# Performance work log

Hardware: AMD Instinct MI355X
Metric: run time of the kernel (lower is better)

Reference implementation:

```python
import jax, jax.numpy as jnp
import numpy as np

R = 32  # voxel resolution
B, CIN, COUT, N = 4, 64, 64, 4096
K = 3


def setup_inputs():
    key = jax.random.key(0)
    ks = jax.random.split(key, 8)
    s = 0.05
    return {
        "features": jax.random.normal(ks[0], (B, CIN, N), jnp.float32),
        "coords": jax.random.normal(ks[1], (B, 3, N), jnp.float32),
        # voxel branch: conv3d + BN x2
        "w1": jax.random.normal(ks[2], (COUT, CIN, K, K, K), jnp.float32) * s,
        "b1": jnp.zeros((COUT,), jnp.float32),
        "g1": jnp.ones((COUT,), jnp.float32),
        "be1": jnp.zeros((COUT,), jnp.float32),
        "w2": jax.random.normal(ks[3], (COUT, COUT, K, K, K), jnp.float32) * s,
        "b2": jnp.zeros((COUT,), jnp.float32),
        "g2": jnp.ones((COUT,), jnp.float32),
        "be2": jnp.zeros((COUT,), jnp.float32),
        # point branch SharedMLP (1x1 conv + BN + ReLU)
        "wp": jax.random.normal(ks[4], (COUT, CIN), jnp.float32) * s,
        "bp": jnp.zeros((COUT,), jnp.float32),
        "gp": jnp.ones((COUT,), jnp.float32),
        "bep": jnp.zeros((COUT,), jnp.float32),
        # fuzzy_proj 1x1 conv
        "wf": jax.random.normal(ks[5], (COUT, CIN), jnp.float32) * s,
        "bf": jnp.zeros((COUT,), jnp.float32),
        # fusion SharedMLP (3*COUT -> COUT)
        "wfu": jax.random.normal(ks[6], (COUT, 3 * COUT), jnp.float32) * s,
        "bfu": jnp.zeros((COUT,), jnp.float32),
        "gfu": jnp.ones((COUT,), jnp.float32),
        "befu": jnp.zeros((COUT,), jnp.float32),
    }


def _bn3d(x, g, b):
    # training-mode BatchNorm3d, eps=1e-4 (biased variance, as torch)
    m = x.mean((0, 2, 3, 4), keepdims=True)
    v = x.var((0, 2, 3, 4), keepdims=True)
    return (x - m) * jax.lax.rsqrt(v + 1e-4) * g[None, :, None, None, None] + b[None, :, None, None, None]


def _bn1d(x, g, b):
    m = x.mean((0, 2), keepdims=True)
    v = x.var((0, 2), keepdims=True)
    return (x - m) * jax.lax.rsqrt(v + 1e-4) * g[None, :, None] + b[None, :, None]


def _conv3d(x, w, b):
    pad = K // 2
    y = jax.lax.conv_general_dilated(x, w, (1, 1, 1), [(pad, pad)] * 3,
                                     dimension_numbers=('NCDHW', 'OIDHW', 'NCDHW'))
    return y + b[None, :, None, None, None]


def _conv1x1(x, w, b):
    return jnp.einsum('oc,bcn->bon', w, x) + b[None, :, None]


def _voxelize(features, coords):
    # PVCNN Voxelization(normalize=True, eps=0): center, scale to unit, grid coords in [0, R-1]
    nc = coords - coords.mean(axis=2, keepdims=True)              # [B,3,N]
    norm = jnp.linalg.norm(nc, axis=1, keepdims=True)             # [B,1,N]
    nc = nc / (norm.max(axis=2, keepdims=True) * 2.0) + 0.5
    nc = jnp.clip(nc * R, 0.0, R - 1)
    vox = jnp.round(nc).astype(jnp.int32)                         # [B,3,N]
    b_, c_, n_ = features.shape
    idx = (vox[:, 0] * R + vox[:, 1]) * R + vox[:, 2]             # [B,N]
    flat = (idx + jnp.arange(b_)[:, None] * R ** 3).reshape(-1)
    feat = features.transpose(0, 2, 1).reshape(b_ * n_, c_)
    sums = jax.ops.segment_sum(feat, flat, num_segments=b_ * R ** 3)
    cnt = jax.ops.segment_sum(jnp.ones((b_ * n_,), feat.dtype), flat, num_segments=b_ * R ** 3)
    avg = sums / jnp.maximum(cnt, 1.0)[:, None]                   # scatter-mean
    grid = avg.reshape(b_, R ** 3, c_).transpose(0, 2, 1).reshape(b_, c_, R, R, R)
    return grid, nc


def _devoxelize(grid, nc):
    # trilinear gather: grid [B,C,R,R,R], nc [B,3,N] float coords in [0,R-1]
    b_, c_ = grid.shape[:2]
    g = grid.reshape(b_, c_, -1)
    lo_f = jnp.floor(nc)
    fr = nc - lo_f                                                # fractional part [B,3,N]
    lo = lo_f.astype(jnp.int32)
    hi = jnp.minimum(lo + 1, R - 1)
    out = jnp.zeros((b_, c_, nc.shape[2]), grid.dtype)
    for dx in (0, 1):
        for dy in (0, 1):
            for dz in (0, 1):
                ix = hi[:, 0] if dx else lo[:, 0]
                iy = hi[:, 1] if dy else lo[:, 1]
                iz = hi[:, 2] if dz else lo[:, 2]
                w = ((fr[:, 0] if dx else 1.0 - fr[:, 0]) *
                     (fr[:, 1] if dy else 1.0 - fr[:, 1]) *
                     (fr[:, 2] if dz else 1.0 - fr[:, 2]))        # [B,N]
                flat = (ix * R + iy) * R + iz                     # [B,N]
                vals = jnp.take_along_axis(g, flat[:, None, :], axis=2)  # [B,C,N]
                out = out + vals * w[:, None, :]
    return out


def reference(features, coords, w1, b1, g1, be1, w2, b2, g2, be2,
              wp, bp, gp, bep, wf, bf, wfu, bfu, gfu, befu):
    lrelu = lambda x: jnp.where(x > 0, x, 0.1 * x)
    # voxel branch
    grid, nc = _voxelize(features, coords)
    v = lrelu(_bn3d(_conv3d(grid, w1, b1), g1, be1))
    v = lrelu(_bn3d(_conv3d(v, w2, b2), g2, be2))
    vox_feat = _devoxelize(v, nc)                                 # [B,COUT,N]
    # point branch
    pt = jax.nn.relu(_bn1d(_conv1x1(features, wp, bp), gp, bep))
    # fuzzy branch: dense attention over points
    cn = coords.transpose(0, 2, 1)                                # [B,N,3]
    cn = cn / jnp.maximum(jnp.linalg.norm(cn, axis=-1, keepdims=True), 1e-12)
    att = jax.nn.softmax(jnp.einsum('bnd,bmd->bnm', cn, cn) / 0.1, axis=-1)
    fz = jnp.einsum('bnm,bcm->bcn', att, features)                # [B,CIN,N]
    fz = _conv1x1(fz, wf, bf)
    # fusion
    comb = jnp.concatenate([vox_feat, pt, fz], axis=1)            # [B,3*COUT,N]
    fused = jax.nn.relu(_bn1d(_conv1x1(comb, wfu, bfu), gfu, befu))
    return (fused, coords)
```

## Files before the change

### kernel.cpp

```cpp
#include <hip/hip_runtime.h>
#include <hip/hip_bf16.h>
#include <math.h>

#define RR 32
#define R3 32768
#define BB 4
#define CI 64
#define CO 64
#define NN 4096

typedef short v8s __attribute__((ext_vector_type(8)));
typedef float v4f __attribute__((ext_vector_type(4)));
typedef unsigned short ushort_t;

__device__ __forceinline__ unsigned short f2bf(float f) {
    unsigned int u = __float_as_uint(f);
    unsigned int r = (u + 0x7FFFu + ((u >> 16) & 1u)) >> 16;
    return (unsigned short)r;
}
__device__ __forceinline__ float bf2f(unsigned short h) {
    return __uint_as_float((unsigned int)h << 16);
}

__device__ __forceinline__ void gll16(const void* g, void* l) {
// ... 126 lines not shown
    }
}

__global__ void k_scan1(const int* __restrict__ cntI, int* __restrict__ lscan,
                        int* __restrict__ bsum, int* __restrict__ rank) {
    __shared__ int sm[256];
    int tid = threadIdx.x;
    int i = blockIdx.x * 256 + tid;
    rank[i] = 0;
    int v = cntI[i];
    sm[tid] = v; __syncthreads();
    for (int off = 1; off < 256; off <<= 1) {
        int t = (tid >= off) ? sm[tid - off] : 0;
        __syncthreads();
        sm[tid] += t;
        __syncthreads();
    }
    lscan[i] = sm[tid] - v;
    if (tid == 255) bsum[blockIdx.x] = sm[tid];
}

__global__ void k_scan2(const int* __restrict__ bsum, int* __restrict__ bbase) {
    __shared__ int sm[512];
    int tid = threadIdx.x;
    int v = bsum[tid];
    sm[tid] = v; __syncthreads();
    for (int off = 1; off < 512; off <<= 1) {
        int t = (tid >= off) ? sm[tid - off] : 0;
        __syncthreads();
        sm[tid] += t;
        __syncthreads();
    }
    bbase[tid] = sm[tid] - v;
}

__global__ void k_fill(const int* __restrict__ vidx, const int* __restrict__ lscan,
                       const int* __restrict__ bbase, int* __restrict__ rank,
                       int* __restrict__ plist) {
    int i = blockIdx.x * 256 + threadIdx.x;
    int b = i >> 12, n = i & (NN - 1);
    int flat = b * R3 + vidx[i];
    int r = atomicAdd(&rank[flat], 1);
    plist[bbase[flat >> 8] + lscan[flat] + r] = n;
}

__global__ __launch_bounds__(256) void k_gather(const float* __restrict__ featT,
                                                const int* __restrict__ cntI,
                                                const int* __restrict__ lscan,
                                                const int* __restrict__ bbase,
                                                const int* __restrict__ plist,
                                                ushort_t* __restrict__ gT) {
    int wv = threadIdx.x >> 6, lane = threadIdx.x & 63;
    int vbase = blockIdx.x * 32 + wv * 8;
    for (int k = 0; k < 8; k++) {
        int flat = vbase + k;
        int count = cntI[flat];
        float s = 0.0f;
        if (count > 0) {
            int b = flat >> 15;
            int start = bbase[flat >> 8] + lscan[flat];
            for (int j = 0; j < count; j++) {
                int n = plist[start + j];
                s += featT[((size_t)b * NN + n) * 64 + lane];
            }
            s *= 1.0f / (float)count;
        }
        gT[(size_t)flat * 64 + lane] = f2bf(s);
    }
}

__global__ void k_bncast2(const ushort_t* __restrict__ x, const float* __restrict__ accs,
                          const float* __restrict__ g, const float* __restrict__ be,
                          float invcnt, float slope, ushort_t* __restrict__ o) {
    size_t i = (size_t)blockIdx.x * 256 + threadIdx.x;
    int c0 = (int)((i * 8) & 63);
    float sc[8], sh[8];
    #pragma unroll
    for (int j = 0; j < 8; j++) {
        int c = c0 + j;
        float mean = accs[2 * c] * invcnt;
        float var = accs[2 * c + 1] * invcnt - mean * mean;
        float scale = g[c] * rsqrtf(var + 1e-4f);
        sc[j] = scale;
        sh[j] = be[c] - mean * scale;
    }
    uint4 in = ((const uint4*)x)[i];
    unsigned iv[4] = {in.x, in.y, in.z, in.w};
    unsigned pk[4];
    #pragma unroll
    for (int j = 0; j < 4; j++) {
        float u0 = bf2f((unsigned short)(iv[j] & 0xFFFF)) * sc[2 * j] + sh[2 * j];
        float u1 = bf2f((unsigned short)(iv[j] >> 16)) * sc[2 * j + 1] + sh[2 * j + 1];
        u0 = u0 > 0 ? u0 : slope * u0;
        u1 = u1 > 0 ? u1 : slope * u1;
        pk[j] = (unsigned)f2bf(u0) | ((unsigned)f2bf(u1) << 16);
    }
    ((uint4*)o)[i] = make_uint4(pk[0], pk[1], pk[2], pk[3]);
}

template <int OUTBF16>
__global__ __launch_bounds__(256) void k_convlds(const ushort_t* __restrict__ gT,
                                                 const ushort_t* __restrict__ wS,
                                                 void* __restrict__ outP,
                                                 float* __restrict__ accs) {
    __shared__ ushort_t lin[20480];
    __shared__ ushort_t lw[2][6144];
    int bid = blockIdx.x;
    int wgid = (bid & 7) * 64 + (bid >> 3);
    int yt = wgid & 3, z0 = (wgid >> 2) & 31, b = wgid >> 7;
    int tid = threadIdx.x;
    int w = __builtin_amdgcn_readfirstlane(tid >> 6);
    int lane = tid & 63, l15 = lane & 15, l4 = lane >> 4;
    int y0 = yt * 8;
    const ushort_t* gTb = gT + (size_t)b * R3 * 64;

    int voxF[4];
    #pragma unroll
    for (int f = 0; f < 4; f++)
        voxF[f] = (w * 2 + (f >> 1)) * 32 + (f & 1) * 16 + l15 - 1;
    bool xlo_ok = (l15 != 0), xhi_ok = (l15 != 15);

    int lsw = lane ^ ((lane >> 3) & 7);
    int wsz8 = ((l15 * 4 + l4) ^ ((l15 >> 1) & 7)) * 8;

    const v8s vzero = {};
    v4f acc[4][4];
    #pragma unroll
    for (int m = 0; m < 4; m++)
        #pragma unroll
        for (int f = 0; f < 4; f++)
            acc[m][f] = (v4f){0.0f, 0.0f, 0.0f, 0.0f};

#define WSTAGE(s)                                                              \
    do {                                                                       \
        const ushort_t* _src = wS + (size_t)(s) * 6144;                        \
        ushort_t* _dst = lw[(s) & 1];                                          \
        _Pragma("unroll") for (int _i = 0; _i < 3; _i++) {                     \
            int _pb = _i * 256 + w * 64;                                       \
            gll16(_src + (size_t)(_pb + lsw) * 8, _dst + (size_t)(_pb + lane) * 8); \
        }                                                                      \
    } while (0)

#define ISTAGE(dz)                                                             \
    do {                                                                       \
        int _zp = z0 - 1 + (dz);                                               \
        if (_zp < 0 || _zp > 31) {                                             \
            for (int _q = 0; _q < 10; _q++)                                    \
                *(v8s*)&lin[(size_t)(w * 640 + _q * 64 + lane) * 8] = vzero;   \
        } else {                                                               \
            if (yt == 0) *(v8s*)&lin[(size_t)tid * 8] = vzero;                 \
            if (yt == 3) *(v8s*)&lin[(size_t)(2304 + tid) * 8] = vzero;        \
            const ushort_t* _pb = gTb + ((size_t)_zp * 1024 + (size_t)(y0 - 1) * 32) * 64; \
            int _g0 = (yt == 0) ? 256 : 0;                                     \
            int _nc = 10 - (yt == 0) - (yt == 3);                              \
            for (int _i = 0; _i < _nc; _i++) {                                 \
                int _pbase = _g0 + _i * 256 + w * 64;                          \
                int _p = _pbase + lane;                                        \
                int _vx = _p >> 3, _js = _p & 7;                               \
                int _sg = _vx * 8 + (_js ^ (_vx & 7));                         \
                gll16(_pb + (size_t)_sg * 8, lin + (size_t)_pbase * 8);        \
            }                                                                  \
        }                                                                      \
    } while (0)

    WSTAGE(0);
    for (int s = 0; s < 18; s++) {
        int dy = (s / 2) % 3, cih = s & 1;
        asm volatile("s_barrier" ::: "memory");
        if ((s % 6) == 0) ISTAGE(s / 6);
        if (s + 1 < 18) WSTAGE(s + 1);
        if (s + 1 < 18) asm volatile("s_waitcnt vmcnt(3) lgkmcnt(0)" ::: "memory");
        else            asm volatile("s_waitcnt vmcnt(0) lgkmcnt(0)" ::: "memory");
        asm volatile("s_barrier" ::: "memory");

        const ushort_t* lwb = lw[s & 1];
        #pragma unroll
        for (int dx = 0; dx < 3; dx++) {
            v8s Bf[4];
            #pragma unroll
            for (int f = 0; f < 4; f++) {
                int vox = voxF[f] + dy * 32 + dx;
                int g = vox * 8 + ((cih * 4 + l4) ^ (vox & 7));
                int bix = g * 16;
                bix = bix < 0 ? 0 : bix;
                v8s vb = *(const v8s*)((const char*)lin + bix);
                bool ok = (dx == 0 && (f & 1) == 0) ? xlo_ok :
                          (dx == 2 && (f & 1) == 1) ? xhi_ok : true;
                Bf[f] = ok ? vb : vzero;
            }
            const ushort_t* ap = lwb + dx * 2048 + wsz8;
            #pragma unroll
            for (int m = 0; m < 4; m++) {
                v8s Af = *(const v8s*)(ap + m * 512);
                #pragma unroll
                for (int f = 0; f < 4; f++)
                    acc[m][f] = __builtin_amdgcn_mfma_f32_16x16x32_bf16(Af, Bf[f], acc[m][f], 0, 0, 0);
            }
        }
    }

    #pragma unroll
    for (int m = 0; m < 4; m++) {
        #pragma unroll
        for (int f = 0; f < 4; f++) {
            int y = y0 + w * 2 + (f >> 1);
            int x = (f & 1) * 16 + l15;
            size_t base = ((size_t)b * R3 + z0 * 1024 + y * 32 + x) * 64 + m * 16 + l4 * 4;
            if (OUTBF16) {
                unsigned p0 = (unsigned)f2bf(acc[m][f][0]) | ((unsigned)f2bf(acc[m][f][1]) << 16);
                unsigned p1 = (unsigned)f2bf(acc[m][f][2]) | ((unsigned)f2bf(acc[m][f][3]) << 16);
                *(uint2*)&((ushort_t*)outP)[base] = make_uint2(p0, p1);
            } else {
                float4 o = make_float4(acc[m][f][0], acc[m][f][1], acc[m][f][2], acc[m][f][3]);
                *(float4*)&((float*)outP)[base] = o;
            }
        }
    }

    __syncthreads();
    float* sbuf = (float*)lin;
    #pragma unroll
    for (int m = 0; m < 4; m++)
        #pragma unroll
        for (int r = 0; r < 4; r++) {
            float s = 0, q = 0;
            #pragma unroll
            for (int f = 0; f < 4; f++) {
                float v = acc[m][f][r];
                s += v; q += v * v;
            }
            sbuf[tid * 33 + (m * 4 + r) * 2] = s;
            sbuf[tid * 33 + (m * 4 + r) * 2 + 1] = q;
        }
    __syncthreads();
    if (tid < 128) {
        int co = tid >> 1, val = tid & 1;
        int m = co >> 4, cl4 = (co >> 2) & 3, r = co & 3;
        float a = 0;
        for (int w2 = 0; w2 < 4; w2++)
            for (int l = 0; l < 16; l++)
                a += sbuf[(w2 * 64 + cl4 * 16 + l) * 33 + (m * 4 + r) * 2 + val];
        atomicAdd(&accs[2 * co + val], a);
    }
#undef WSTAGE
#undef ISTAGE
}

__global__ void k_bnfin2(const float* __restrict__ pst, const float* __restrict__ g,
                         const float* __restrict__ be, float* __restrict__ stats,
                         float invcnt) {
    int c = blockIdx.x, tid = threadIdx.x;
    __shared__ float rs[256], rq[256];
    rs[tid] = pst[(c * 256 + tid) * 2];
    rq[tid] = pst[(c * 256 + tid) * 2 + 1];
    __syncthreads();
    for (int off = 128; off > 0; off >>= 1) {
        if (tid < off) { rs[tid] += rs[tid + off]; rq[tid] += rq[tid + off]; }
        __syncthreads();
    }
    if (tid == 0) {
        float mean = rs[0] * invcnt;
        float var = rq[0] * invcnt - mean * mean;
        float sc = g[c] * rsqrtf(var + 1e-4f);
        stats[2 * c] = sc;
        stats[2 * c + 1] = be[c] - mean * sc;
    }
}

__global__ void k_bnact2(const float* __restrict__ x, const float* __restrict__ pst,
                         const float* __restrict__ g, const float* __restrict__ be,
                         float invcnt, float* __restrict__ out) {
    int bid = blockIdx.x, tid = threadIdx.x;
    int c = (bid >> 2) & 63;
    __shared__ float rs[256], rq[256];
    __shared__ float sscale, sshift;
    rs[tid] = pst[(c * 256 + tid) * 2];
    rq[tid] = pst[(c * 256 + tid) * 2 + 1];
    __syncthreads();
    for (int off = 128; off > 0; off >>= 1) {
        if (tid < off) { rs[tid] += rs[tid + off]; rq[tid] += rq[tid + off]; }
        __syncthreads();
    }
    if (tid == 0) {
        float mean = rs[0] * invcnt;
        float var = rq[0] * invcnt - mean * mean;
        float sc = g[c] * rsqrtf(var + 1e-4f);
        sscale = sc;
        sshift = be[c] - mean * sc;
    }
    __syncthreads();
    float sc = sscale, sh = sshift;
    size_t i = (size_t)bid * 256 + tid;
    float4 v = ((const float4*)x)[i];
    v.x = fmaxf(v.x * sc + sh, 0.0f);
    v.y = fmaxf(v.y * sc + sh, 0.0f);
    v.z = fmaxf(v.z * sc + sh, 0.0f);
    v.w = fmaxf(v.w * sc + sh, 0.0f);
    ((float4*)out)[i] = v;
}

__global__ void k_devox2(const ushort_t* __restrict__ gcl, const float* __restrict__ accs,
                         const float* __restrict__ g, const float* __restrict__ be,
                         float invcnt, const float* __restrict__ nc,
                         float* __restrict__ out) {
    int b = blockIdx.y;
    int tid = threadIdx.x, p = tid >> 4, q = tid & 15;
    int n = blockIdx.x * 16 + p;
    float x = nc[((size_t)b * 3 + 0) * NN + n];
    float y = nc[((size_t)b * 3 + 1) * NN + n];
    float z = nc[((size_t)b * 3 + 2) * NN + n];
    float fx = floorf(x), fy = floorf(y), fz = floorf(z);
    int lx = (int)fx, ly = (int)fy, lz = (int)fz;
    int hx = min(lx + 1, RR - 1), hy = min(ly + 1, RR - 1), hz = min(lz + 1, RR - 1);
    float frx = x - fx, fry = y - fy, frz = z - fz;
    int xx[2] = {lx, hx}, yy[2] = {ly, hy}, zz[2] = {lz, hz};
    float wx[2] = {1.0f - frx, frx}, wy[2] = {1.0f - fry, fry}, wz[2] = {1.0f - frz, frz};
    float sc[4], sh[4];
    #pragma unroll
    for (int j = 0; j < 4; j++) {
        int c = q * 4 + j;
        float mean = accs[2 * c] * invcnt;
        float var = accs[2 * c + 1] * invcnt - mean * mean;
        float scale = g[c] * rsqrtf(var + 1e-4f);
        sc[j] = scale;
        sh[j] = be[c] - mean * scale;
    }
    float a0 = 0, a1 = 0, a2 = 0, a3 = 0;
    #pragma unroll
    for (int dx = 0; dx < 2; dx++)
        #pragma unroll
        for (int dy = 0; dy < 2; dy++)
            #pragma unroll
            for (int dz = 0; dz < 2; dz++) {
                int idx = (xx[dx] * RR + yy[dy]) * RR + zz[dz];
                float wt = wx[dx] * wy[dy] * wz[dz];
                uint2 pv = *(const uint2*)&gcl[((size_t)b * R3 + idx) * 64 + q * 4];
                float v0 = bf2f((unsigned short)(pv.x & 0xFFFF));
                float v1 = bf2f((unsigned short)(pv.x >> 16));
                float v2 = bf2f((unsigned short)(pv.y & 0xFFFF));
                float v3 = bf2f((unsigned short)(pv.y >> 16));
                float u0 = v0 * sc[0] + sh[0]; u0 = u0 > 0 ? u0 : 0.1f * u0;
                float u1 = v1 * sc[1] + sh[1]; u1 = u1 > 0 ? u1 : 0.1f * u1;
                float u2 = v2 * sc[2] + sh[2]; u2 = u2 > 0 ? u2 : 0.1f * u2;
                float u3 = v3 * sc[3] + sh[3]; u3 = u3 > 0 ? u3 : 0.1f * u3;
                a0 += wt * u0; a1 += wt * u1; a2 += wt * u2; a3 += wt * u3;
            }
    out[((size_t)(b * 64 + q * 4 + 0)) * NN + n] = a0;
    out[((size_t)(b * 64 + q * 4 + 1)) * NN + n] = a1;
    out[((size_t)(b * 64 + q * 4 + 2)) * NN + n] = a2;
    out[((size_t)(b * 64 + q * 4 + 3)) * NN + n] = a3;
}

__global__ __launch_bounds__(256) void k_fuzzym(const float* __restrict__ coords,
                                                const ushort_t* __restrict__ featb,
                                                float* __restrict__ pnum,
                                                float* __restrict__ pden) {
    __shared__ float cm[3][1024];
    __shared__ ushort_t la[4][2048];
    int b = blockIdx.z, mc = blockIdx.y, nt = blockIdx.x;
    int tid = threadIdx.x;
    int w = tid >> 6, lane = tid & 63, l15 = lane & 15, l4 = lane >> 4;
    int m0 = mc * 1024;

    for (int i = tid; i < 1024; i += 256) {
        float a0 = coords[((size_t)b * 3 + 0) * NN + m0 + i];
        float a1 = coords[((size_t)b * 3 + 1) * NN + m0 + i];
        float a2 = coords[((size_t)b * 3 + 2) * NN + m0 + i];
        float inv = 1.0f / fmaxf(sqrtf(a0 * a0 + a1 * a1 + a2 * a2), 1e-12f);
        cm[0][i] = a0 * inv; cm[1][i] = a1 * inv; cm[2][i] = a2 * inv;
    }

    int n = nt * 64 + w * 16 + l15;
    float q0 = coords[((size_t)b * 3 + 0) * NN + n];
    float q1 = coords[((size_t)b * 3 + 1) * NN + n];
    float q2 = coords[((size_t)b * 3 + 2) * NN + n];
    float qi = 10.0f / fmaxf(sqrtf(q0 * q0 + q1 * q1 + q2 * q2), 1e-12f);
    q0 *= qi; q1 *= qi; q2 *= qi;

    int srow = tid >> 2, sslot = tid & 3;
    int g0 = sslot ^ ((srow >> 1) & 3);
    const ushort_t* fb = featb + (size_t)b * 64 * NN + m0;
    const ushort_t* sbase = fb + (size_t)srow * NN + g0 * 8;
    int rsw = (l15 >> 1) & 3;

    v4f acc[4];
    #pragma unroll
    for (int cb = 0; cb < 4; cb++) acc[cb] = (v4f){0.0f, 0.0f, 0.0f, 0.0f};
    float den = 0.0f;

    gll16(sbase, &la[0][(size_t)tid * 8]);
    gll16(sbase + 32, &la[1][(size_t)tid * 8]);
    gll16(sbase + 64, &la[2][(size_t)tid * 8]);

    for (int t = 0; t < 32; t++) {
        int cur = t & 3;
        asm volatile("s_waitcnt vmcnt(2)" ::: "memory");
        __syncthreads();
        if (t + 3 < 32)
            gll16(sbase + (t + 3) * 32, &la[(t + 3) & 3][(size_t)tid * 8]);

        int mo = t * 32 + l4 * 8;
        float e[8];
        #pragma unroll
        for (int jj = 0; jj < 2; jj++) {
            float4 x0 = *(const float4*)&cm[0][mo + jj * 4];
            float4 x1 = *(const float4*)&cm[1][mo + jj * 4];
            float4 x2 = *(const float4*)&cm[2][mo + jj * 4];
            e[jj * 4 + 0] = __expf(q0 * x0.x + q1 * x1.x + q2 * x2.x);
            e[jj * 4 + 1] = __expf(q0 * x0.y + q1 * x1.y + q2 * x2.y);
            e[jj * 4 + 2] = __expf(q0 * x0.z + q1 * x1.z + q2 * x2.z);
            e[jj * 4 + 3] = __expf(q0 * x0.w + q1 * x1.w + q2 * x2.w);
        }
        den += ((e[0] + e[1]) + (e[2] + e[3])) + ((e[4] + e[5]) + (e[6] + e[7]));
        union { __hip_bfloat162 h[4]; v8s v; } pk;
        pk.h[0] = __float22bfloat162_rn(make_float2(e[0], e[1]));
        pk.h[1] = __float22bfloat162_rn(make_float2(e[2], e[3]));
        pk.h[2] = __float22bfloat162_rn(make_float2(e[4], e[5]));
        pk.h[3] = __float22bfloat162_rn(make_float2(e[6], e[7]));
        #pragma unroll
        for (int cb = 0; cb < 4; cb++) {
            v8s A = *(const v8s*)&la[cur][(size_t)((cb * 16 + l15) * 4 + (l4 ^ rsw)) * 8];
            acc[cb] = __builtin_amdgcn_mfma_f32_16x16x32_bf16(A, pk.v, acc[cb], 0, 0, 0);
        }
    }

    den += __shfl_xor(den, 16);
    den += __shfl_xor(den, 32);

    size_t obase = ((size_t)(b * 4 + mc)) * 64 * NN;
    #pragma unroll
    for (int cb = 0; cb < 4; cb++)
        #pragma unroll
        for (int r = 0; r < 4; r++)
            pnum[obase + (size_t)(cb * 16 + l4 * 4 + r) * NN + n] = acc[cb][r];
    if (l4 == 0) pden[((size_t)(b * 4 + mc)) * NN + n] = den;
}

__global__ void k_combine2(const float* __restrict__ pnum, const float* __restrict__ pden,
                           float* __restrict__ fzf) {
    int i4 = blockIdx.x * 256 + threadIdx.x;
    int b = i4 >> 16, c = (i4 >> 10) & 63, n4 = i4 & 1023;
    float4 num = make_float4(0, 0, 0, 0), den = make_float4(0, 0, 0, 0);
    #pragma unroll
    for (int ch = 0; ch < 4; ch++) {
        float4 pn = ((const float4*)pnum)[((size_t)(b * 4 + ch) * 64 + c) * 1024 + n4];
        float4 pd = ((const float4*)pden)[(size_t)(b * 4 + ch) * 1024 + n4];
        num.x += pn.x; num.y += pn.y; num.z += pn.z; num.w += pn.w;
        den.x += pd.x; den.y += pd.y; den.z += pd.z; den.w += pd.w;
    }
    float4 o = make_float4(num.x / den.x, num.y / den.y, num.z / den.z, num.w / den.w);
    ((float4*)fzf)[((size_t)(b * 64 + c)) * 1024 + n4] = o;
}

__global__ __launch_bounds__(256) void k_1x1s(const float* __restrict__ in,
                                              const float* __restrict__ wT,
                                              const float* __restrict__ bias,
                                              float* __restrict__ out,
                                              float* __restrict__ pst) {
    int b = blockIdx.z, ob = blockIdx.y, bx = blockIdx.x;
    int tid = threadIdx.x;
    int q = tid & 15, o = ob * 16 + (tid >> 4);
    int n = bx * 64 + q * 4;
    const float* src = in + (size_t)b * 64 * NN + n;
    const float* wp_ = wT + o;
    v4f acc = {0, 0, 0, 0};
    #pragma unroll 8
    for (int c = 0; c < 64; c++) {
        float4 x = *(const float4*)&src[(size_t)c * NN];
        float w = wp_[c * 64];
        acc[0] += x.x * w; acc[1] += x.y * w; acc[2] += x.z * w; acc[3] += x.w * w;
    }
    float bv = bias[o];
    float s = 0, q2 = 0;
    float4 ov;
    float* op = (float*)&ov;
    #pragma unroll
    for (int v = 0; v < 4; v++) {
        float val = acc[v] + bv;
        op[v] = val;
        s += val; q2 += val * val;
    }
    *(float4*)&out[((size_t)(b * 64 + o)) * NN + n] = ov;
    #pragma unroll
    for (int off = 1; off < 16; off <<= 1) {
        s += __shfl_xor(s, off);
        q2 += __shfl_xor(q2, off);
    }
    if (q == 0) {
        int part = bx * 4 + b;
        pst[(o * 256 + part) * 2] = s;
        pst[(o * 256 + part) * 2 + 1] = q2;
    }
}

__global__ __launch_bounds__(256) void k_1x1f(const float* __restrict__ vox,
                                              const float* __restrict__ pt,
                                              const float* __restrict__ fzf,
                                              const float* __restrict__ bnB,
                                              const float* __restrict__ wfuT,
                                              const float* __restrict__ bC,
                                              float* __restrict__ out,
                                              float* __restrict__ pst) {
    int b = blockIdx.z, ob = blockIdx.y, bx = blockIdx.x;
    int tid = threadIdx.x;
    int q = tid & 15, o = ob * 16 + (tid >> 4);
    int n = bx * 64 + q * 4;
    const float* srcA = vox + (size_t)b * 64 * NN + n;
    const float* srcB = pt + (size_t)b * 64 * NN + n;
    const float* srcC = fzf + (size_t)b * 64 * NN + n;
    const float* wA = wfuT + o;
    v4f acc = {0, 0, 0, 0};
    #pragma unroll 8
    for (int c = 0; c < 64; c++) {
        float4 x = *(const float4*)&srcA[(size_t)c * NN];
        float w = wA[c * 64];
        acc[0] += x.x * w; acc[1] += x.y * w; acc[2] += x.z * w; acc[3] += x.w * w;
    }
    #pragma unroll 8
    for (int c = 0; c < 64; c++) {
        float4 x = *(const float4*)&srcB[(size_t)c * NN];
        float sc = bnB[2 * c], sh = bnB[2 * c + 1];
        float w = wA[(64 + c) * 64];
        float x0 = fmaxf(x.x * sc + sh, 0.0f), x1 = fmaxf(x.y * sc + sh, 0.0f);
        float x2 = fmaxf(x.z * sc + sh, 0.0f), x3 = fmaxf(x.w * sc + sh, 0.0f);
        acc[0] += x0 * w; acc[1] += x1 * w; acc[2] += x2 * w; acc[3] += x3 * w;
    }
    #pragma unroll 8
    for (int c = 0; c < 64; c++) {
        float4 x = *(const float4*)&srcC[(size_t)c * NN];
        float w = wA[(128 + c) * 64];
        acc[0] += x.x * w; acc[1] += x.y * w; acc[2] += x.z * w; acc[3] += x.w * w;
    }
    float bv = bC[o];
    float s = 0, q2 = 0;
    float4 ov;
    float* op = (float*)&ov;
    #pragma unroll
    for (int v = 0; v < 4; v++) {
        float val = acc[v] + bv;
        op[v] = val;
        s += val; q2 += val * val;
    }
    *(float4*)&out[((size_t)(b * 64 + o)) * NN + n] = ov;
    #pragma unroll
    for (int off = 1; off < 16; off <<= 1) {
        s += __shfl_xor(s, off);
        q2 += __shfl_xor(q2, off);
    }
    if (q == 0) {
        int part = bx * 4 + b;
        pst[(o * 256 + part) * 2] = s;
        pst[(o * 256 + part) * 2 + 1] = q2;
    }
}

extern "C" void kernel_launch(void* const* d_in, const int* in_sizes, int n_in,
                              void* d_out, int out_size, void* d_ws, size_t ws_size,
                              hipStream_t stream) {
    const float* features = (const float*)d_in[0];
    const float* coords = (const float*)d_in[1];
    const float* w1 = (const float*)d_in[2];
    const float* g1 = (const float*)d_in[4];
    const float* be1 = (const float*)d_in[5];
    const float* w2 = (const float*)d_in[6];
    const float* g2 = (const float*)d_in[8];
    const float* be2 = (const float*)d_in[9];
    const float* wp = (const float*)d_in[10];
    const float* bp = (const float*)d_in[11];
    const float* gp = (const float*)d_in[12];
    const float* bep = (const float*)d_in[13];
    const float* wf = (const float*)d_in[14];
    const float* bf = (const float*)d_in[15];
    const float* wfu = (const float*)d_in[16];
    const float* bfu = (const float*)d_in[17];
    const float* gfu = (const float*)d_in[18];
    const float* befu = (const float*)d_in[19];

    float* ws = (float*)d_ws;
    float* nc = ws;
    int* vidx = (int*)(ws + 49152);
    int* cntI = (int*)(ws + 65536);
    float* pden = ws + 65536;
    float* gridCL = ws + 196608;
    ushort_t* gTraw = (ushort_t*)gridCL;
    int* rank = (int*)(ws + 196608);
    int* lscan = (int*)(ws + 327680);
    int* bsum = (int*)(ws + 458752);
    int* bbase = (int*)(ws + 459264);
    int* plist = (int*)(ws + 459776);
    float* featT = ws + 476160;
    float* gTpool = ws + 8585216;
    ushort_t* gT = (ushort_t*)gTpool;
    float* pnum = gTpool;
    float* pstB = gTpool + 4194304;
    float* stats = ws + 16973824;
    float* voxreg = ws + 16974336;
    ushort_t* wS1 = (ushort_t*)voxreg;
    ushort_t* wS2 = wS1 + 110592;
    float* vox = voxreg;
    float* pt = ws + 18022912;
    float* fzf = ws + 19071488;
    float* wpT = ws + 20120064;
    float* wfuT = wpT + 4096;
    float* bC = wfuT + 12288;
    float* fpre = ws + 21168640;
    ushort_t* featb = (ushort_t*)fpre;
    float* accs = ws + 22217216;

    float* out = (float*)d_out;

    k_prep<<<1699, 256, 0, stream>>>(wp, wfu, wf, bf, bfu, wpT, wfuT, bC, accs,
                                     w1, w2, wS1, wS2, features, featT, featb, cntI);

    k_nc<<<BB, 256, 0, stream>>>(coords, nc, vidx, cntI);
    k_scan1<<<512, 256, 0, stream>>>(cntI, lscan, bsum, rank);
    k_scan2<<<1, 512, 0, stream>>>(bsum, bbase);
    k_fill<<<BB * NN / 256, 256, 0, stream>>>(vidx, lscan, bbase, rank, plist);
    k_gather<<<4096, 256, 0, stream>>>(featT, cntI, lscan, bbase, plist, gT);

    k_convlds<1><<<512, 256, 0, stream>>>(gT, wS1, gTraw, accs);
    k_bncast2<<<BB * R3 * 64 / 8 / 256, 256, 0, stream>>>(gTraw, accs, g1, be1,
                                                          1.0f / (BB * R3), 0.1f, gT);
    k_convlds<1><<<512, 256, 0, stream>>>(gT, wS2, gTraw, accs + 128);
    k_devox2<<<dim3(NN / 16, BB), 256, 0, stream>>>(gTraw, accs + 128, g2, be2,
                                                    1.0f / (BB * R3), nc, vox);

    k_fuzzym<<<dim3(64, 4, BB), 256, 0, stream>>>(coords, featb, pnum, pden);
    k_combine2<<<BB * 64 * NN / 4 / 256, 256, 0, stream>>>(pnum, pden, fzf);

    k_1x1s<<<dim3(NN / 64, 4, BB), 256, 0, stream>>>(features, wpT, bp, pt, pstB);
    k_bnfin2<<<64, 256, 0, stream>>>(pstB, gp, bep, stats + 256, 1.0f / (BB * NN));

    k_1x1f<<<dim3(NN / 64, 4, BB), 256, 0, stream>>>(vox, pt, fzf, stats + 256, wfuT, bC,
                                                     fpre, pstB);
    k_bnact2<<<BB * 64 * NN / 4 / 256, 256, 0, stream>>>(fpre, pstB, gfu, befu,
                                                         1.0f / (BB * NN), out);

    hipMemcpyAsync(out + (size_t)BB * CO * NN, coords, (size_t)BB * 3 * NN * 4,
                   hipMemcpyDeviceToDevice, stream);
}
```

Measured before the change: 256.6 us.

## Merge independent mid-stage kernels into block-dispatched launches and fold coords copy

Devoxelize, fuzzy attention and point-branch 1x1 conv are merged into one launch that picks its branch from the block index. Fuzzy combine and point BN finalize share another launch, and the coords output copy moves into the final BN-activation kernel in place of a separate memcpy. This removes several launch gaps and lets the independent branches run concurrently on the GPU. The cost is a uniform shared-memory allocation across all branches, which can lower occupancy for the lighter branches, plus uneven work per block.

Measured after the change: 237.3 us. 1.08x faster.

```diff
diff --git a/kernel.cpp b/kernel.cpp
--- a/kernel.cpp
+++ b/kernel.cpp
@@ -302,7 +302,7 @@
             if (yt == 3) *(v8s*)&lin[(size_t)(2304 + tid) * 8] = vzero;        \
             const ushort_t* _pb = gTb + ((size_t)_zp * 1024 + (size_t)(y0 - 1) * 32) * 64; \
             int _g0 = (yt == 0) ? 256 : 0;                                     \
-            int _nc = 10 - (yt == 0) - (yt == 3);                              \
+            int _nc = 10 - (yt == 0) - (yt == 3);                               \
             for (int _i = 0; _i < _nc; _i++) {                                 \
                 int _pbase = _g0 + _i * 256 + w * 64;                          \
                 int _p = _pbase + lane;                                        \
@@ -396,250 +396,218 @@
 #undef ISTAGE
 }
 
-__global__ void k_bnfin2(const float* __restrict__ pst, const float* __restrict__ g,
-                         const float* __restrict__ be, float* __restrict__ stats,
-                         float invcnt) {
-    int c = blockIdx.x, tid = threadIdx.x;
-    __shared__ float rs[256], rq[256];
-    rs[tid] = pst[(c * 256 + tid) * 2];
-    rq[tid] = pst[(c * 256 + tid) * 2 + 1];
-    __syncthreads();
-    for (int off = 128; off > 0; off >>= 1) {
-        if (tid < off) { rs[tid] += rs[tid + off]; rq[tid] += rq[tid + off]; }
-        __syncthreads();
-    }
-    if (tid == 0) {
-        float mean = rs[0] * invcnt;
-        float var = rq[0] * invcnt - mean * mean;
-        float sc = g[c] * rsqrtf(var + 1e-4f);
-        stats[2 * c] = sc;
-        stats[2 * c + 1] = be[c] - mean * sc;
-    }
-}
-
-__global__ void k_bnact2(const float* __restrict__ x, const float* __restrict__ pst,
-                         const float* __restrict__ g, const float* __restrict__ be,
-                         float invcnt, float* __restrict__ out) {
-    int bid = blockIdx.x, tid = threadIdx.x;
-    int c = (bid >> 2) & 63;
-    __shared__ float rs[256], rq[256];
-    __shared__ float sscale, sshift;
-    rs[tid] = pst[(c * 256 + tid) * 2];
-    rq[tid] = pst[(c * 256 + tid) * 2 + 1];
-    __syncthreads();
-    for (int off = 128; off > 0; off >>= 1) {
-        if (tid < off) { rs[tid] += rs[tid + off]; rq[tid] += rq[tid + off]; }
-        __syncthreads();
-    }
-    if (tid == 0) {
-        float mean = rs[0] * invcnt;
-        float var = rq[0] * invcnt - mean * mean;
-        float sc = g[c] * rsqrtf(var + 1e-4f);
-        sscale = sc;
-        sshift = be[c] - mean * sc;
-    }
-    __syncthreads();
-    float sc = sscale, sh = sshift;
-    size_t i = (size_t)bid * 256 + tid;
-    float4 v = ((const float4*)x)[i];
-    v.x = fmaxf(v.x * sc + sh, 0.0f);
-    v.y = fmaxf(v.y * sc + sh, 0.0f);
-    v.z = fmaxf(v.z * sc + sh, 0.0f);
-    v.w = fmaxf(v.w * sc + sh, 0.0f);
-    ((float4*)out)[i] = v;
-}
-
-__global__ void k_devox2(const ushort_t* __restrict__ gcl, const float* __restrict__ accs,
-                         const float* __restrict__ g, const float* __restrict__ be,
-                         float invcnt, const float* __restrict__ nc,
-                         float* __restrict__ out) {
-    int b = blockIdx.y;
-    int tid = threadIdx.x, p = tid >> 4, q = tid & 15;
-    int n = blockIdx.x * 16 + p;
-    float x = nc[((size_t)b * 3 + 0) * NN + n];
-    float y = nc[((size_t)b * 3 + 1) * NN + n];
-    float z = nc[((size_t)b * 3 + 2) * NN + n];
-    float fx = floorf(x), fy = floorf(y), fz = floorf(z);
-    int lx = (int)fx, ly = (int)fy, lz = (int)fz;
-    int hx = min(lx + 1, RR - 1), hy = min(ly + 1, RR - 1), hz = min(lz + 1, RR - 1);
-    float frx = x - fx, fry = y - fy, frz = z - fz;
-    int xx[2] = {lx, hx}, yy[2] = {ly, hy}, zz[2] = {lz, hz};
-    float wx[2] = {1.0f - frx, frx}, wy[2] = {1.0f - fry, fry}, wz[2] = {1.0f - frz, frz};
-    float sc[4], sh[4];
-    #pragma unroll
-    for (int j = 0; j < 4; j++) {
-        int c = q * 4 + j;
-        float mean = accs[2 * c] * invcnt;
-        float var = accs[2 * c + 1] * invcnt - mean * mean;
-        float scale = g[c] * rsqrtf(var + 1e-4f);
-        sc[j] = scale;
-        sh[j] = be[c] - mean * scale;
-    }
-    float a0 = 0, a1 = 0, a2 = 0, a3 = 0;
-    #pragma unroll
-    for (int dx = 0; dx < 2; dx++)
-        #pragma unroll
-        for (int dy = 0; dy < 2; dy++)
-            #pragma unroll
-            for (int dz = 0; dz < 2; dz++) {
-                int idx = (xx[dx] * RR + yy[dy]) * RR + zz[dz];
-                float wt = wx[dx] * wy[dy] * wz[dz];
-                uint2 pv = *(const uint2*)&gcl[((size_t)b * R3 + idx) * 64 + q * 4];
-                float v0 = bf2f((unsigned short)(pv.x & 0xFFFF));
-                float v1 = bf2f((unsigned short)(pv.x >> 16));
-                float v2 = bf2f((unsigned short)(pv.y & 0xFFFF));
-                float v3 = bf2f((unsigned short)(pv.y >> 16));
-                float u0 = v0 * sc[0] + sh[0]; u0 = u0 > 0 ? u0 : 0.1f * u0;
-                float u1 = v1 * sc[1] + sh[1]; u1 = u1 > 0 ? u1 : 0.1f * u1;
-                float u2 = v2 * sc[2] + sh[2]; u2 = u2 > 0 ? u2 : 0.1f * u2;
-                float u3 = v3 * sc[3] + sh[3]; u3 = u3 > 0 ? u3 : 0.1f * u3;
-                a0 += wt * u0; a1 += wt * u1; a2 += wt * u2; a3 += wt * u3;
-            }
-    out[((size_t)(b * 64 + q * 4 + 0)) * NN + n] = a0;
-    out[((size_t)(b * 64 + q * 4 + 1)) * NN + n] = a1;
-    out[((size_t)(b * 64 + q * 4 + 2)) * NN + n] = a2;
-    out[((size_t)(b * 64 + q * 4 + 3)) * NN + n] = a3;
-}
-
-__global__ __launch_bounds__(256) void k_fuzzym(const float* __restrict__ coords,
-                                                const ushort_t* __restrict__ featb,
-                                                float* __restrict__ pnum,
-                                                float* __restrict__ pden) {
+__global__ __launch_bounds__(256) void k_mid(
+        const ushort_t* __restrict__ gcl, const float* __restrict__ accs2,
+        const float* __restrict__ g2, const float* __restrict__ be2, float invcntR3,
+        const float* __restrict__ nc, float* __restrict__ vox,
+        const float* __restrict__ coords, const ushort_t* __restrict__ featb,
+        float* __restrict__ pnum, float* __restrict__ pden,
+        const float* __restrict__ features, const float* __restrict__ wpT,
+        const float* __restrict__ bp, float* __restrict__ pt, float* __restrict__ pstB) {
     __shared__ float cm[3][1024];
     __shared__ ushort_t la[4][2048];
-    int b = blockIdx.z, mc = blockIdx.y, nt = blockIdx.x;
-    int tid = threadIdx.x;
-    int w = tid >> 6, lane = tid & 63, l15 = lane & 15, l4 = lane >> 4;
-    int m0 = mc * 1024;
-
-    for (int i = tid; i < 1024; i += 256) {
-        float a0 = coords[((size_t)b * 3 + 0) * NN + m0 + i];
-        float a1 = coords[((size_t)b * 3 + 1) * NN + m0 + i];
-        float a2 = coords[((size_t)b * 3 + 2) * NN + m0 + i];
-        float inv = 1.0f / fmaxf(sqrtf(a0 * a0 + a1 * a1 + a2 * a2), 1e-12f);
-        cm[0][i] = a0 * inv; cm[1][i] = a1 * inv; cm[2][i] = a2 * inv;
-    }
-
-    int n = nt * 64 + w * 16 + l15;
-    float q0 = coords[((size_t)b * 3 + 0) * NN + n];
-    float q1 = coords[((size_t)b * 3 + 1) * NN + n];
-    float q2 = coords[((size_t)b * 3 + 2) * NN + n];
-    float qi = 10.0f / fmaxf(sqrtf(q0 * q0 + q1 * q1 + q2 * q2), 1e-12f);
-    q0 *= qi; q1 *= qi; q2 *= qi;
-
-    int srow = tid >> 2, sslot = tid & 3;
-    int g0 = sslot ^ ((srow >> 1) & 3);
-    const ushort_t* fb = featb + (size_t)b * 64 * NN + m0;
-    const ushort_t* sbase = fb + (size_t)srow * NN + g0 * 8;
-    int rsw = (l15 >> 1) & 3;
-
-    v4f acc[4];
-    #pragma unroll
-    for (int cb = 0; cb < 4; cb++) acc[cb] = (v4f){0.0f, 0.0f, 0.0f, 0.0f};
-    float den = 0.0f;
-
-    gll16(sbase, &la[0][(size_t)tid * 8]);
-    gll16(sbase + 32, &la[1][(size_t)tid * 8]);
-    gll16(sbase + 64, &la[2][(size_t)tid * 8]);
-
-    for (int t = 0; t < 32; t++) {
-        int cur = t & 3;
-        asm volatile("s_waitcnt vmcnt(2)" ::: "memory");
-        __syncthreads();
-        if (t + 3 < 32)
-            gll16(sbase + (t + 3) * 32, &la[(t + 3) & 3][(size_t)tid * 8]);
-
-        int mo = t * 32 + l4 * 8;
-        float e[8];
-        #pragma unroll
-        for (int jj = 0; jj < 2; jj++) {
-            float4 x0 = *(const float4*)&cm[0][mo + jj * 4];
-            float4 x1 = *(const float4*)&cm[1][mo + jj * 4];
-            float4 x2 = *(const float4*)&cm[2][mo + jj * 4];
-            e[jj * 4 + 0] = __expf(q0 * x0.x + q1 * x1.x + q2 * x2.x);
-            e[jj * 4 + 1] = __expf(q0 * x0.y + q1 * x1.y + q2 * x2.y);
-            e[jj * 4 + 2] = __expf(q0 * x0.z + q1 * x1.z + q2 * x2.z);
-            e[jj * 4 + 3] = __expf(q0 * x0.w + q1 * x1.w + q2 * x2.w);
-        }
-        den += ((e[0] + e[1]) + (e[2] + e[3])) + ((e[4] + e[5]) + (e[6] + e[7]));
-        union { __hip_bfloat162 h[4]; v8s v; } pk;
-        pk.h[0] = __float22bfloat162_rn(make_float2(e[0], e[1]));
-        pk.h[1] = __float22bfloat162_rn(make_float2(e[2], e[3]));
-        pk.h[2] = __float22bfloat162_rn(make_float2(e[4], e[5]));
-        pk.h[3] = __float22bfloat162_rn(make_float2(e[6], e[7]));
-        #pragma unroll
-        for (int cb = 0; cb < 4; cb++) {
-            v8s A = *(const v8s*)&la[cur][(size_t)((cb * 16 + l15) * 4 + (l4 ^ rsw)) * 8];
-            acc[cb] = __builtin_amdgcn_mfma_f32_16x16x32_bf16(A, pk.v, acc[cb], 0, 0, 0);
-        }
-    }
-
-    den += __shfl_xor(den, 16);
-    den += __shfl_xor(den, 32);
-
-    size_t obase = ((size_t)(b * 4 + mc)) * 64 * NN;
-    #pragma unroll
-    for (int cb = 0; cb < 4; cb++)
-        #pragma unroll
-        for (int r = 0; r < 4; r++)
-            pnum[obase + (size_t)(cb * 16 + l4 * 4 + r) * NN + n] = acc[cb][r];
-    if (l4 == 0) pden[((size_t)(b * 4 + mc)) * NN + n] = den;
-}
-
-__global__ void k_combine2(const float* __restrict__ pnum, const float* __restrict__ pden,
-                           float* __restrict__ fzf) {
-    int i4 = blockIdx.x * 256 + threadIdx.x;
-    int b = i4 >> 16, c = (i4 >> 10) & 63, n4 = i4 & 1023;
-    float4 num = make_float4(0, 0, 0, 0), den = make_float4(0, 0, 0, 0);
-    #pragma unroll
-    for (int ch = 0; ch < 4; ch++) {
-        float4 pn = ((const float4*)pnum)[((size_t)(b * 4 + ch) * 64 + c) * 1024 + n4];
-        float4 pd = ((const float4*)pden)[(size_t)(b * 4 + ch) * 1024 + n4];
-        num.x += pn.x; num.y += pn.y; num.z += pn.z; num.w += pn.w;
-        den.x += pd.x; den.y += pd.y; den.z += pd.z; den.w += pd.w;
-    }
-    float4 o = make_float4(num.x / den.x, num.y / den.y, num.z / den.z, num.w / den.w);
-    ((float4*)fzf)[((size_t)(b * 64 + c)) * 1024 + n4] = o;
-}
-
-__global__ __launch_bounds__(256) void k_1x1s(const float* __restrict__ in,
-                                              const float* __restrict__ wT,
-                                              const float* __restrict__ bias,
-                                              float* __restrict__ out,
-                                              float* __restrict__ pst) {
-    int b = blockIdx.z, ob = blockIdx.y, bx = blockIdx.x;
-    int tid = threadIdx.x;
-    int q = tid & 15, o = ob * 16 + (tid >> 4);
-    int n = bx * 64 + q * 4;
-    const float* src = in + (size_t)b * 64 * NN + n;
-    const float* wp_ = wT + o;
-    v4f acc = {0, 0, 0, 0};
-    #pragma unroll 8
-    for (int c = 0; c < 64; c++) {
-        float4 x = *(const float4*)&src[(size_t)c * NN];
-        float w = wp_[c * 64];
-        acc[0] += x.x * w; acc[1] += x.y * w; acc[2] += x.z * w; acc[3] += x.w * w;
-    }
-    float bv = bias[o];
-    float s = 0, q2 = 0;
-    float4 ov;
-    float* op = (float*)&ov;
-    #pragma unroll
-    for (int v = 0; v < 4; v++) {
-        float val = acc[v] + bv;
-        op[v] = val;
-        s += val; q2 += val * val;
-    }
-    *(float4*)&out[((size_t)(b * 64 + o)) * NN + n] = ov;
-    #pragma unroll
-    for (int off = 1; off < 16; off <<= 1) {
-        s += __shfl_xor(s, off);
-        q2 += __shfl_xor(q2, off);
-    }
-    if (q == 0) {
-        int part = bx * 4 + b;
-        pst[(o * 256 + part) * 2] = s;
-        pst[(o * 256 + part) * 2 + 1] = q2;
+    int bid0 = blockIdx.x, tid = threadIdx.x;
+
+    if (bid0 < 1024) {
+        int b = bid0 >> 8;
+        int nblk = bid0 & 255;
+        int p = tid >> 4, q = tid & 15;
+        int n = nblk * 16 + p;
+        float x = nc[((size_t)b * 3 + 0) * NN + n];
+        float y = nc[((size_t)b * 3 + 1) * NN + n];
+        float z = nc[((size_t)b * 3 + 2) * NN + n];
+        float fx = floorf(x), fy = floorf(y), fz = floorf(z);
+        int lx = (int)fx, ly = (int)fy, lz = (int)fz;
+        int hx = min(lx + 1, RR - 1), hy = min(ly + 1, RR - 1), hz = min(lz + 1, RR - 1);
+        float frx = x - fx, fry = y - fy, frz = z - fz;
+        int xx[2] = {lx, hx}, yy[2] = {ly, hy}, zz[2] = {lz, hz};
+        float wx[2] = {1.0f - frx, frx}, wy[2] = {1.0f - fry, fry}, wz[2] = {1.0f - frz, frz};
+        float sc[4], sh[4];
+        #pragma unroll
+        for (int j = 0; j < 4; j++) {
+            int c = q * 4 + j;
+            float mean = accs2[2 * c] * invcntR3;
+            float var = accs2[2 * c + 1] * invcntR3 - mean * mean;
+            float scale = g2[c] * rsqrtf(var + 1e-4f);
+            sc[j] = scale;
+            sh[j] = be2[c] - mean * scale;
+        }
+        float a0 = 0, a1 = 0, a2 = 0, a3 = 0;
+        #pragma unroll
+        for (int dx = 0; dx < 2; dx++)
+            #pragma unroll
+            for (int dy = 0; dy < 2; dy++)
+                #pragma unroll
+                for (int dz = 0; dz < 2; dz++) {
+                    int idx = (xx[dx] * RR + yy[dy]) * RR + zz[dz];
+                    float wt = wx[dx] * wy[dy] * wz[dz];
+                    uint2 pv = *(const uint2*)&gcl[((size_t)b * R3 + idx) * 64 + q * 4];
+                    float v0 = bf2f((unsigned short)(pv.x & 0xFFFF));
+                    float v1 = bf2f((unsigned short)(pv.x >> 16));
+                    float v2 = bf2f((unsigned short)(pv.y & 0xFFFF));
+                    float v3 = bf2f((unsigned short)(pv.y >> 16));
+                    float u0 = v0 * sc[0] + sh[0]; u0 = u0 > 0 ? u0 : 0.1f * u0;
+                    float u1 = v1 * sc[1] + sh[1]; u1 = u1 > 0 ? u1 : 0.1f * u1;
+                    float u2 = v2 * sc[2] + sh[2]; u2 = u2 > 0 ? u2 : 0.1f * u2;
+                    float u3 = v3 * sc[3] + sh[3]; u3 = u3 > 0 ? u3 : 0.1f * u3;
+                    a0 += wt * u0; a1 += wt * u1; a2 += wt * u2; a3 += wt * u3;
+                }
+        vox[((size_t)(b * 64 + q * 4 + 0)) * NN + n] = a0;
+        vox[((size_t)(b * 64 + q * 4 + 1)) * NN + n] = a1;
+        vox[((size_t)(b * 64 + q * 4 + 2)) * NN + n] = a2;
+        vox[((size_t)(b * 64 + q * 4 + 3)) * NN + n] = a3;
+    } else if (bid0 < 2048) {
+        int pb = bid0 - 1024;
+        int nt = pb & 63, mc = (pb >> 6) & 3, b = pb >> 8;
+        int w = tid >> 6, lane = tid & 63, l15 = lane & 15, l4 = lane >> 4;
+        int m0 = mc * 1024;
+
+        for (int i = tid; i < 1024; i += 256) {
+            float a0 = coords[((size_t)b * 3 + 0) * NN + m0 + i];
+            float a1 = coords[((size_t)b * 3 + 1) * NN + m0 + i];
+            float a2 = coords[((size_t)b * 3 + 2) * NN + m0 + i];
+            float inv = 1.0f / fmaxf(sqrtf(a0 * a0 + a1 * a1 + a2 * a2), 1e-12f);
+            cm[0][i] = a0 * inv; cm[1][i] = a1 * inv; cm[2][i] = a2 * inv;
+        }
+
+        int n = nt * 64 + w * 16 + l15;
+        float q0 = coords[((size_t)b * 3 + 0) * NN + n];
+        float q1 = coords[((size_t)b * 3 + 1) * NN + n];
+        float q2 = coords[((size_t)b * 3 + 2) * NN + n];
+        float qi = 10.0f / fmaxf(sqrtf(q0 * q0 + q1 * q1 + q2 * q2), 1e-12f);
+        q0 *= qi; q1 *= qi; q2 *= qi;
+
+        int srow = tid >> 2, sslot = tid & 3;
+        int g0 = sslot ^ ((srow >> 1) & 3);
+        const ushort_t* fb = featb + (size_t)b * 64 * NN + m0;
+        const ushort_t* sbase = fb + (size_t)srow * NN + g0 * 8;
+        int rsw = (l15 >> 1) & 3;
+
+        v4f acc[4];
+        #pragma unroll
+        for (int cb = 0; cb < 4; cb++) acc[cb] = (v4f){0.0f, 0.0f, 0.0f, 0.0f};
+        float den = 0.0f;
+
+        gll16(sbase, &la[0][(size_t)tid * 8]);
+        gll16(sbase + 32, &la[1][(size_t)tid * 8]);
+        gll16(sbase + 64, &la[2][(size_t)tid * 8]);
+
+        for (int t = 0; t < 32; t++) {
+            int cur = t & 3;
+            asm volatile("s_waitcnt vmcnt(2)" ::: "memory");
+            __syncthreads();
+            if (t + 3 < 32)
+                gll16(sbase + (t + 3) * 32, &la[(t + 3) & 3][(size_t)tid * 8]);
+
+            int mo = t * 32 + l4 * 8;
+            float e[8];
+            #pragma unroll
+            for (int jj = 0; jj < 2; jj++) {
+                float4 x0 = *(const float4*)&cm[0][mo + jj * 4];
+                float4 x1 = *(const float4*)&cm[1][mo + jj * 4];
+                float4 x2 = *(const float4*)&cm[2][mo + jj * 4];
+                e[jj * 4 + 0] = __expf(q0 * x0.x + q1 * x1.x + q2 * x2.x);
+                e[jj * 4 + 1] = __expf(q0 * x0.y + q1 * x1.y + q2 * x2.y);
+                e[jj * 4 + 2] = __expf(q0 * x0.z + q1 * x1.z + q2 * x2.z);
+                e[jj * 4 + 3] = __expf(q0 * x0.w + q1 * x1.w + q2 * x2.w);
+            }
+            den += ((e[0] + e[1]) + (e[2] + e[3])) + ((e[4] + e[5]) + (e[6] + e[7]));
+            union { __hip_bfloat162 h[4]; v8s v; } pk;
+            pk.h[0] = __float22bfloat162_rn(make_float2(e[0], e[1]));
+            pk.h[1] = __float22bfloat162_rn(make_float2(e[2], e[3]));
+            pk.h[2] = __float22bfloat162_rn(make_float2(e[4], e[5]));
+            pk.h[3] = __float22bfloat162_rn(make_float2(e[6], e[7]));
+            #pragma unroll
+            for (int cb = 0; cb < 4; cb++) {
+                v8s A = *(const v8s*)&la[cur][(size_t)((cb * 16 + l15) * 4 + (l4 ^ rsw)) * 8];
+                acc[cb] = __builtin_amdgcn_mfma_f32_16x16x32_bf16(A, pk.v, acc[cb], 0, 0, 0);
+            }
+        }
+
+        den += __shfl_xor(den, 16);
+        den += __shfl_xor(den, 32);
+
+        size_t obase = ((size_t)(b * 4 + mc)) * 64 * NN;
+        #pragma unroll
+        for (int cb = 0; cb < 4; cb++)
+            #pragma unroll
+            for (int r = 0; r < 4; r++)
+                pnum[obase + (size_t)(cb * 16 + l4 * 4 + r) * NN + n] = acc[cb][r];
+        if (l4 == 0) pden[((size_t)(b * 4 + mc)) * NN + n] = den;
+    } else {
+        int pb = bid0 - 2048;
+        int bx = pb & 63, ob = (pb >> 6) & 3, b = pb >> 8;
+        int q = tid & 15, o = ob * 16 + (tid >> 4);
+        int n = bx * 64 + q * 4;
+        const float* src = features + (size_t)b * 64 * NN + n;
+        const float* wp_ = wpT + o;
+        v4f acc = {0, 0, 0, 0};
+        #pragma unroll 8
+        for (int c = 0; c < 64; c++) {
+            float4 x = *(const float4*)&src[(size_t)c * NN];
+            float w = wp_[c * 64];
+            acc[0] += x.x * w; acc[1] += x.y * w; acc[2] += x.z * w; acc[3] += x.w * w;
+        }
+        float bv = bp[o];
+        float s = 0, q2 = 0;
+        float4 ov;
+        float* op = (float*)&ov;
+        #pragma unroll
+        for (int v = 0; v < 4; v++) {
+            float val = acc[v] + bv;
+            op[v] = val;
+            s += val; q2 += val * val;
+        }
+        *(float4*)&pt[((size_t)(b * 64 + o)) * NN + n] = ov;
+        #pragma unroll
+        for (int off = 1; off < 16; off <<= 1) {
+            s += __shfl_xor(s, off);
+            q2 += __shfl_xor(q2, off);
+        }
+        if (q == 0) {
+            int part = bx * 4 + b;
+            pstB[(o * 256 + part) * 2] = s;
+            pstB[(o * 256 + part) * 2 + 1] = q2;
+        }
+    }
+}
+
+__global__ void k_fin(const float* __restrict__ pnum, const float* __restrict__ pden,
+                      float* __restrict__ fzf,
+                      const float* __restrict__ pst, const float* __restrict__ g,
+                      const float* __restrict__ be, float* __restrict__ stats,
+                      float invcnt) {
+    __shared__ float rs[256], rq[256];
+    int bid = blockIdx.x, tid = threadIdx.x;
+    if (bid < 1024) {
+        int i4 = bid * 256 + tid;
+        int b = i4 >> 16, c = (i4 >> 10) & 63, n4 = i4 & 1023;
+        float4 num = make_float4(0, 0, 0, 0), den = make_float4(0, 0, 0, 0);
+        #pragma unroll
+        for (int ch = 0; ch < 4; ch++) {
+            float4 pn = ((const float4*)pnum)[((size_t)(b * 4 + ch) * 64 + c) * 1024 + n4];
+            float4 pd = ((const float4*)pden)[(size_t)(b * 4 + ch) * 1024 + n4];
+            num.x += pn.x; num.y += pn.y; num.z += pn.z; num.w += pn.w;
+            den.x += pd.x; den.y += pd.y; den.z += pd.z; den.w += pd.w;
+        }
+        float4 o = make_float4(num.x / den.x, num.y / den.y, num.z / den.z, num.w / den.w);
+        ((float4*)fzf)[((size_t)(b * 64 + c)) * 1024 + n4] = o;
+    } else {
+        int c = bid - 1024;
+        rs[tid] = pst[(c * 256 + tid) * 2];
+        rq[tid] = pst[(c * 256 + tid) * 2 + 1];
+        __syncthreads();
+        for (int off = 128; off > 0; off >>= 1) {
+            if (tid < off) { rs[tid] += rs[tid + off]; rq[tid] += rq[tid + off]; }
+            __syncthreads();
+        }
+        if (tid == 0) {
+            float mean = rs[0] * invcnt;
+            float var = rq[0] * invcnt - mean * mean;
+            float sc = g[c] * rsqrtf(var + 1e-4f);
+            stats[2 * c] = sc;
+            stats[2 * c + 1] = be[c] - mean * sc;
+        }
     }
 }
 
@@ -702,6 +670,44 @@
         pst[(o * 256 + part) * 2] = s;
         pst[(o * 256 + part) * 2 + 1] = q2;
     }
+}
+
+__global__ void k_bnact2(const float* __restrict__ x, const float* __restrict__ pst,
+                         const float* __restrict__ g, const float* __restrict__ be,
+                         float invcnt, float* __restrict__ out,
+                         const float* __restrict__ coords, float* __restrict__ outc) {
+    int bid = blockIdx.x, tid = threadIdx.x;
+    if (bid >= 1024) {
+        int i4 = (bid - 1024) * 256 + tid;
+        ((float4*)outc)[i4] = ((const float4*)coords)[i4];
+        return;
+    }
+    int c = (bid >> 2) & 63;
+    __shared__ float rs[256], rq[256];
+    __shared__ float sscale, sshift;
+    rs[tid] = pst[(c * 256 + tid) * 2];
+    rq[tid] = pst[(c * 256 + tid) * 2 + 1];
+    __syncthreads();
+    for (int off = 128; off > 0; off >>= 1) {
+        if (tid < off) { rs[tid] += rs[tid + off]; rq[tid] += rq[tid + off]; }
+        __syncthreads();
+    }
+    if (tid == 0) {
+        float mean = rs[0] * invcnt;
+        float var = rq[0] * invcnt - mean * mean;
+        float sc = g[c] * rsqrtf(var + 1e-4f);
+        sscale = sc;
+        sshift = be[c] - mean * sc;
+    }
+    __syncthreads();
+    float sc = sscale, sh = sshift;
+    size_t i = (size_t)bid * 256 + tid;
+    float4 v = ((const float4*)x)[i];
+    v.x = fmaxf(v.x * sc + sh, 0.0f);
+    v.y = fmaxf(v.y * sc + sh, 0.0f);
+    v.z = fmaxf(v.z * sc + sh, 0.0f);
+    v.w = fmaxf(v.w * sc + sh, 0.0f);
+    ((float4*)out)[i] = v;
 }
 
 extern "C" void kernel_launch(void* const* d_in, const int* in_sizes, int n_in,
@@ -772,20 +778,16 @@
     k_bncast2<<<BB * R3 * 64 / 8 / 256, 256, 0, stream>>>(gTraw, accs, g1, be1,
                                                           1.0f / (BB * R3), 0.1f, gT);
     k_convlds<1><<<512, 256, 0, stream>>>(gT, wS2, gTraw, accs + 128);
-    k_devox2<<<dim3(NN / 16, BB), 256, 0, stream>>>(gTraw, accs + 128, g2, be2,
-                                                    1.0f / (BB * R3), nc, vox);
-
-    k_fuzzym<<<dim3(64, 4, BB), 256, 0, stream>>>(coords, featb, pnum, pden);
-    k_combine2<<<BB * 64 * NN / 4 / 256, 256, 0, stream>>>(pnum, pden, fzf);
-
-    k_1x1s<<<dim3(NN / 64, 4, BB), 256, 0, stream>>>(features, wpT, bp, pt, pstB);
-    k_bnfin2<<<64, 256, 0, stream>>>(pstB, gp, bep, stats + 256, 1.0f / (BB * NN));
+
+    k_mid<<<3072, 256, 0, stream>>>(gTraw, accs + 128, g2, be2, 1.0f / (BB * R3), nc, vox,
+                                    coords, featb, pnum, pden,
+                                    features, wpT, bp, pt, pstB);
+
+    k_fin<<<1088, 256, 0, stream>>>(pnum, pden, fzf, pstB, gp, bep, stats + 256,
+                                    1.0f / (BB * NN));
 
     k_1x1f<<<dim3(NN / 64, 4, BB), 256, 0, stream>>>(vox, pt, fzf, stats + 256, wfuT, bC,
                                                      fpre, pstB);
-    k_bnact2<<<BB * 64 * NN / 4 / 256, 256, 0, stream>>>(fpre, pstB, gfu, befu,
-                                                         1.0f / (BB * NN), out);
-
-    hipMemcpyAsync(out + (size_t)BB * CO * NN, coords, (size_t)BB * 3 * NN * 4,
-                   hipMemcpyDeviceToDevice, stream);
-}
+    k_bnact2<<<1072, 256, 0, stream>>>(fpre, pstB, gfu, befu, 1.0f / (BB * NN), out,
+                                       coords, out + (size_t)BB * CO * NN);
+}
```
